# Performance work log

Measured on AMD Instinct MI355X. Metric: run time of the kernel, lower is better.

The kernel has to match this reference:

```python
import jax, jax.numpy as jnp
import numpy as np

IN_F = 4096
OUT_F = 4096
GROUP = 8
N_GROUPS = OUT_F * IN_F // GROUP  # 2097152
BATCH = 32


def _dequant_3bit(weight_q3, weight_norm):
    # weight_q3: [G, 3] bytes (stored int32, values 0..255)
    # weight_norm: [G, 1] fp16 per-group abs-max scale
    p = weight_q3.astype(jnp.int32)
    val = p[:, 0] | (p[:, 1] << 8) | (p[:, 2] << 16)          # [G] 24-bit word
    shifts = jnp.arange(GROUP, dtype=jnp.int32) * 3           # [8]
    q = ((val[:, None] >> shifts[None, :]) & 7).astype(jnp.float32)  # [G, 8] in {0..7}
    n = weight_norm.astype(jnp.float32)                        # [G, 1]
    w = (q / 7.0) * (2.0 * n) - n                              # de-normalize to [-n, n]
    return w.reshape(OUT_F, IN_F)


def setup_inputs() -> dict:
    key = jax.random.key(0)
    k1, k2, k3, k4 = jax.random.split(key, 4)
    x = jax.random.normal(k1, (BATCH, IN_F), dtype=jnp.float32)
    weight_q3 = jax.random.randint(k2, (N_GROUPS, 3), 0, 256, dtype=jnp.int32)
    weight_norm = jax.random.uniform(k3, (N_GROUPS, 1), dtype=jnp.float16, minval=0.01, maxval=1.0)
    bias = jax.random.normal(k4, (OUT_F,), dtype=jnp.float32)
    return {"x": x, "weight_q3": weight_q3, "weight_norm": weight_norm, "bias": bias}


def reference(x, weight_q3, weight_norm, bias):
    w = _dequant_3bit(weight_q3, weight_norm)  # [OUT_F, IN_F] fp32
    return x @ w.T + bias                      # F.linear semantics
```

## Files before the change

kernel.cpp:

```cpp
#include <hip/hip_runtime.h>
#include <hip/hip_fp16.h>

#define IN_F   4096
#define OUT_F  4096
#define BATCH  32
#define NGPR   512
#define BN     16
#define NW     8
#define QPITCH 1540
#define NPITCH 516

typedef float f32x4  __attribute__((ext_vector_type(4)));
typedef short short8 __attribute__((ext_vector_type(8)));

__device__ __forceinline__ unsigned short f2bf_u(float f) {
    return __builtin_bit_cast(unsigned short, (__bf16)f);
}

__device__ __forceinline__ void gload16(const void* gsrc, void* lds) {
    __builtin_amdgcn_global_load_lds(
        (const __attribute__((address_space(1))) void*)gsrc,
        (__attribute__((address_space(3))) void*)lds, 16, 0, 0);
}

__global__ __launch_bounds__(256)
void pack_x_kernel(const float* __restrict__ x, unsigned short* __restrict__ apk)
{
    const int tau = blockIdx.x * 256 + threadIdx.x;
    const int row = tau >> 9;
    const int c   = tau & 511;
    const float4 lo = *reinterpret_cast<const float4*>(&x[row * IN_F + c * 8]);
    const float4 hi = *reinterpret_cast<const float4*>(&x[row * IN_F + c * 8 + 4]);
    union { unsigned short us[8]; uint4 v; } pk;
    pk.us[0] = f2bf_u(lo.x); pk.us[1] = f2bf_u(lo.y);
    pk.us[2] = f2bf_u(lo.z); pk.us[3] = f2bf_u(lo.w);
    pk.us[4] = f2bf_u(hi.x); pk.us[5] = f2bf_u(hi.y);
    pk.us[6] = f2bf_u(hi.z); pk.us[7] = f2bf_u(hi.w);
    const int a = row >> 4, cl = row & 15, s = c >> 2, q = c & 3;
    const int unit = (a * 128 + s) * 64 + q * 16 + cl;
    *reinterpret_cast<uint4*>(&apk[unit * 8]) = pk.v;
}

template<bool PACKED>
__global__ __launch_bounds__(512, 2)
void l3b_main(const float* __restrict__ x,
              const int* __restrict__ wq3,
              const void* __restrict__ wnorm_raw,
              const float* __restrict__ bias,
              float* __restrict__ out,
              const unsigned short* __restrict__ apk)
{
    __shared__ unsigned int qls[BN * QPITCH];
    __shared__ float        nrm[BN][NPITCH];
    __shared__ float        red[NW][BATCH][17];

    const int tid   = threadIdx.x;
    const int w     = tid >> 6;
    const int lane  = tid & 63;
    const int nbase = blockIdx.x * BN;

    const int q  = lane >> 4;
    const int cl = lane & 15;

    const unsigned short* wn16  = (const unsigned short*)wnorm_raw;
    const float*          wn32  = (const float*)wnorm_raw;
    const unsigned int*   wnu32 = (const unsigned int*)wnorm_raw;
    int mode;
    {
        const unsigned short h = wn16[lane];
        const float v16 = __half2float(__builtin_bit_cast(__half, h));
        const float vbf = __builtin_bit_cast(float, (unsigned int)h << 16);
        const float v32 = wn32[lane];
        const int c16 = __popcll(__ballot(v16 > 0.0095f && v16 < 1.0005f));
        const int cbf = __popcll(__ballot(vbf > 0.0095f && vbf < 1.0005f));
        const int c32 = __popcll(__ballot(v32 > 0.0095f && v32 < 1.0005f));
        if (c16 >= c32 && c16 >= cbf) {
            mode = 1;
        } else if (c32 > cbf + 8) {
            mode = 0;
        } else if (cbf > c32 + 8) {
            mode = 2;
        } else {
            const int z = __popcll(__ballot((wnu32[lane] & 0x1FFFu) == 0u));
            mode = (z >= 48) ? 0 : 2;
        }
    }

    {
        const int* qg = wq3 + (long)nbase * 1536;
        #pragma unroll
        for (int rr = 0; rr < 2; ++rr) {
            const int row = w * 2 + rr;
            #pragma unroll
            for (int i = 0; i < 6; ++i) {
                const int off = i * 256 + lane * 4;
                gload16(qg + (long)row * 1536 + off, &qls[row * QPITCH + off]);
            }
        }
    }

    if (mode == 0) {
        const float* nb = wn32 + (long)nbase * NGPR;
        #pragma unroll
        for (int j = 0; j < 4; ++j) {
            const int f = j * 2048 + tid * 4;
            const float4 v = *reinterpret_cast<const float4*>(nb + f);
            *reinterpret_cast<float4*>(&nrm[f >> 9][f & 511]) = v;
        }
    } else {
        const unsigned short* nb = wn16 + (long)nbase * NGPR;
        #pragma unroll
        for (int j = 0; j < 2; ++j) {
            const int f = j * 4096 + tid * 8;
            union { unsigned short us[8]; uint4 v; } u;
            u.v = *reinterpret_cast<const uint4*>(nb + f);
            float4 f0, f1;
            if (mode == 1) {
                f0.x = __half2float(__builtin_bit_cast(__half, u.us[0]));
                f0.y = __half2float(__builtin_bit_cast(__half, u.us[1]));
                f0.z = __half2float(__builtin_bit_cast(__half, u.us[2]));
                f0.w = __half2float(__builtin_bit_cast(__half, u.us[3]));
                f1.x = __half2float(__builtin_bit_cast(__half, u.us[4]));
                f1.y = __half2float(__builtin_bit_cast(__half, u.us[5]));
                f1.z = __half2float(__builtin_bit_cast(__half, u.us[6]));
                f1.w = __half2float(__builtin_bit_cast(__half, u.us[7]));
            } else {
                f0.x = __builtin_bit_cast(float, (unsigned)u.us[0] << 16);
                f0.y = __builtin_bit_cast(float, (unsigned)u.us[1] << 16);
                f0.z = __builtin_bit_cast(float, (unsigned)u.us[2] << 16);
                f0.w = __builtin_bit_cast(float, (unsigned)u.us[3] << 16);
                f1.x = __builtin_bit_cast(float, (unsigned)u.us[4] << 16);
                f1.y = __builtin_bit_cast(float, (unsigned)u.us[5] << 16);
                f1.z = __builtin_bit_cast(float, (unsigned)u.us[6] << 16);
                f1.w = __builtin_bit_cast(float, (unsigned)u.us[7] << 16);
            }
            const int row = f >> 9, col = f & 511;
            *reinterpret_cast<float4*>(&nrm[row][col])     = f0;
            *reinterpret_cast<float4*>(&nrm[row][col + 4]) = f1;
        }
    }

    __syncthreads();

    f32x4 acc0 = {0.f, 0.f, 0.f, 0.f};
    f32x4 acc1 = {0.f, 0.f, 0.f, 0.f};

    #pragma unroll 4
    for (int i = 0; i < 16; ++i) {
        const int s = w * 16 + i;
        const int g = s * 4 + q;

        const int qb = cl * QPITCH + g * 3;
        const unsigned d0 = qls[qb];
        const unsigned d1 = qls[qb + 1];
        const unsigned d2 = qls[qb + 2];
        const unsigned val = (d0 & 0xFFu) | ((d1 & 0xFFu) << 8) | ((d2 & 0xFFu) << 16);

        const float n  = nrm[cl][g];
        const float av = n * 0.285714285714285714f;
        union { unsigned short us[8]; short8 v; } B;
        #pragma unroll
        for (int e = 0; e < 8; ++e) {
            const float qf = (float)((val >> (3 * e)) & 7u);
            B.us[e] = f2bf_u(fmaf(qf, av, -n));
        }

        short8 A0, A1;
        if (PACKED) {
            A0 = *reinterpret_cast<const short8*>(&apk[(s * 64 + lane) * 8]);
            A1 = *reinterpret_cast<const short8*>(&apk[((128 + s) * 64 + lane) * 8]);
        } else {
            const int kg = s * 32 + q * 8;
            const float4 a0lo = *reinterpret_cast<const float4*>(&x[cl        * IN_F + kg]);
            const float4 a0hi = *reinterpret_cast<const float4*>(&x[cl        * IN_F + kg + 4]);
            const float4 a1lo = *reinterpret_cast<const float4*>(&x[(cl + 16) * IN_F + kg]);
            const float4 a1hi = *reinterpret_cast<const float4*>(&x[(cl + 16) * IN_F + kg + 4]);
            union { unsigned short us[8]; short8 v; } U0, U1;
            U0.us[0] = f2bf_u(a0lo.x); U0.us[1] = f2bf_u(a0lo.y);
            U0.us[2] = f2bf_u(a0lo.z); U0.us[3] = f2bf_u(a0lo.w);
            U0.us[4] = f2bf_u(a0hi.x); U0.us[5] = f2bf_u(a0hi.y);
            U0.us[6] = f2bf_u(a0hi.z); U0.us[7] = f2bf_u(a0hi.w);
            U1.us[0] = f2bf_u(a1lo.x); U1.us[1] = f2bf_u(a1lo.y);
            U1.us[2] = f2bf_u(a1lo.z); U1.us[3] = f2bf_u(a1lo.w);
            U1.us[4] = f2bf_u(a1hi.x); U1.us[5] = f2bf_u(a1hi.y);
            U1.us[6] = f2bf_u(a1hi.z); U1.us[7] = f2bf_u(a1hi.w);
            A0 = U0.v; A1 = U1.v;
        }

        acc0 = __builtin_amdgcn_mfma_f32_16x16x32_bf16(A0, B.v, acc0, 0, 0, 0);
        acc1 = __builtin_amdgcn_mfma_f32_16x16x32_bf16(A1, B.v, acc1, 0, 0, 0);
    }

    #pragma unroll
    for (int i = 0; i < 4; ++i) {
        red[w][q * 4 + i][cl]      = acc0[i];
        red[w][16 + q * 4 + i][cl] = acc1[i];
    }
    __syncthreads();
    {
        const int m  = tid >> 4;
        const int nl = tid & 15;
        float ssum = 0.f;
        #pragma unroll
        for (int wv = 0; wv < NW; ++wv) ssum += red[wv][m][nl];
        out[m * OUT_F + nbase + nl] = ssum + bias[nbase + nl];
    }
}

extern "C" void kernel_launch(void* const* d_in, const int* in_sizes, int n_in,
                              void* d_out, int out_size, void* d_ws, size_t ws_size,
                              hipStream_t stream) {
    const float* x    = (const float*)d_in[0];
    const int*   wq3  = (const int*)d_in[1];
    const void*  wn   = (const void*)d_in[2];
    const float* bias = (const float*)d_in[3];
    float*       out  = (float*)d_out;

    if (ws_size >= (size_t)(2 * 128 * 64 * 8 * 2)) {
        unsigned short* apk = (unsigned short*)d_ws;
        pack_x_kernel<<<dim3(64), dim3(256), 0, stream>>>(x, apk);
        l3b_main<true><<<dim3(OUT_F / BN), dim3(512), 0, stream>>>(x, wq3, wn, bias, out, apk);
    } else {
        l3b_main<false><<<dim3(OUT_F / BN), dim3(512), 0, stream>>>(x, wq3, wn, bias, out, nullptr);
    }
}
```

Baseline: 17.22 us.

## Fuse activation bf16 packing into main kernel and prefetch A fragments into registers

Removes the separate pack_x kernel launch and its workspace round trip. Each wave now loads and converts its x slice to bf16 directly into register arrays before the main loop. The load is issued before the barrier so it can overlap the LDS staging of quantized weights. The MFMA loop is then fully unrolled. In exchange, the x conversion is repeated in every block, and holding 32 short8 registers per thread raises register pressure under the 512-thread, 2-blocks launch bound, which may cause spills.

```diff
diff --git a/kernel.cpp b/kernel.cpp
--- a/kernel.cpp
+++ b/kernel.cpp
@@ -23,32 +23,12 @@
         (__attribute__((address_space(3))) void*)lds, 16, 0, 0);
 }
 
-__global__ __launch_bounds__(256)
-void pack_x_kernel(const float* __restrict__ x, unsigned short* __restrict__ apk)
-{
-    const int tau = blockIdx.x * 256 + threadIdx.x;
-    const int row = tau >> 9;
-    const int c   = tau & 511;
-    const float4 lo = *reinterpret_cast<const float4*>(&x[row * IN_F + c * 8]);
-    const float4 hi = *reinterpret_cast<const float4*>(&x[row * IN_F + c * 8 + 4]);
-    union { unsigned short us[8]; uint4 v; } pk;
-    pk.us[0] = f2bf_u(lo.x); pk.us[1] = f2bf_u(lo.y);
-    pk.us[2] = f2bf_u(lo.z); pk.us[3] = f2bf_u(lo.w);
-    pk.us[4] = f2bf_u(hi.x); pk.us[5] = f2bf_u(hi.y);
-    pk.us[6] = f2bf_u(hi.z); pk.us[7] = f2bf_u(hi.w);
-    const int a = row >> 4, cl = row & 15, s = c >> 2, q = c & 3;
-    const int unit = (a * 128 + s) * 64 + q * 16 + cl;
-    *reinterpret_cast<uint4*>(&apk[unit * 8]) = pk.v;
-}
-
-template<bool PACKED>
 __global__ __launch_bounds__(512, 2)
-void l3b_main(const float* __restrict__ x,
-              const int* __restrict__ wq3,
-              const void* __restrict__ wnorm_raw,
-              const float* __restrict__ bias,
-              float* __restrict__ out,
-              const unsigned short* __restrict__ apk)
+void l3b_fused(const float* __restrict__ x,
+               const int* __restrict__ wq3,
+               const void* __restrict__ wnorm_raw,
+               const float* __restrict__ bias,
+               float* __restrict__ out)
 {
     __shared__ unsigned int qls[BN * QPITCH];
     __shared__ float        nrm[BN][NPITCH];
@@ -140,12 +120,33 @@
         }
     }
 
+    short8 A0R[16], A1R[16];
+    #pragma unroll
+    for (int i = 0; i < 16; ++i) {
+        const int kg = (w * 16 + i) * 32 + q * 8;
+        const float4 a0lo = *reinterpret_cast<const float4*>(&x[cl        * IN_F + kg]);
+        const float4 a0hi = *reinterpret_cast<const float4*>(&x[cl        * IN_F + kg + 4]);
+        const float4 a1lo = *reinterpret_cast<const float4*>(&x[(cl + 16) * IN_F + kg]);
+        const float4 a1hi = *reinterpret_cast<const float4*>(&x[(cl + 16) * IN_F + kg + 4]);
+        union { unsigned short us[8]; short8 v; } U0, U1;
+        U0.us[0] = f2bf_u(a0lo.x); U0.us[1] = f2bf_u(a0lo.y);
+        U0.us[2] = f2bf_u(a0lo.z); U0.us[3] = f2bf_u(a0lo.w);
+        U0.us[4] = f2bf_u(a0hi.x); U0.us[5] = f2bf_u(a0hi.y);
+        U0.us[6] = f2bf_u(a0hi.z); U0.us[7] = f2bf_u(a0hi.w);
+        U1.us[0] = f2bf_u(a1lo.x); U1.us[1] = f2bf_u(a1lo.y);
+        U1.us[2] = f2bf_u(a1lo.z); U1.us[3] = f2bf_u(a1lo.w);
+        U1.us[4] = f2bf_u(a1hi.x); U1.us[5] = f2bf_u(a1hi.y);
+        U1.us[6] = f2bf_u(a1hi.z); U1.us[7] = f2bf_u(a1hi.w);
+        A0R[i] = U0.v;
+        A1R[i] = U1.v;
+    }
+
     __syncthreads();
 
     f32x4 acc0 = {0.f, 0.f, 0.f, 0.f};
     f32x4 acc1 = {0.f, 0.f, 0.f, 0.f};
 
-    #pragma unroll 4
+    #pragma unroll
     for (int i = 0; i < 16; ++i) {
         const int s = w * 16 + i;
         const int g = s * 4 + q;
@@ -165,30 +166,8 @@
             B.us[e] = f2bf_u(fmaf(qf, av, -n));
         }
 
-        short8 A0, A1;
-        if (PACKED) {
-            A0 = *reinterpret_cast<const short8*>(&apk[(s * 64 + lane) * 8]);
-            A1 = *reinterpret_cast<const short8*>(&apk[((128 + s) * 64 + lane) * 8]);
-        } else {
-            const int kg = s * 32 + q * 8;
-            const float4 a0lo = *reinterpret_cast<const float4*>(&x[cl        * IN_F + kg]);
-            const float4 a0hi = *reinterpret_cast<const float4*>(&x[cl        * IN_F + kg + 4]);
-            const float4 a1lo = *reinterpret_cast<const float4*>(&x[(cl + 16) * IN_F + kg]);
-            const float4 a1hi = *reinterpret_cast<const float4*>(&x[(cl + 16) * IN_F + kg + 4]);
-            union { unsigned short us[8]; short8 v; } U0, U1;
-            U0.us[0] = f2bf_u(a0lo.x); U0.us[1] = f2bf_u(a0lo.y);
-            U0.us[2] = f2bf_u(a0lo.z); U0.us[3] = f2bf_u(a0lo.w);
-            U0.us[4] = f2bf_u(a0hi.x); U0.us[5] = f2bf_u(a0hi.y);
-            U0.us[6] = f2bf_u(a0hi.z); U0.us[7] = f2bf_u(a0hi.w);
-            U1.us[0] = f2bf_u(a1lo.x); U1.us[1] = f2bf_u(a1lo.y);
-            U1.us[2] = f2bf_u(a1lo.z); U1.us[3] = f2bf_u(a1lo.w);
-            U1.us[4] = f2bf_u(a1hi.x); U1.us[5] = f2bf_u(a1hi.y);
-            U1.us[6] = f2bf_u(a1hi.z); U1.us[7] = f2bf_u(a1hi.w);
-            A0 = U0.v; A1 = U1.v;
-        }
-
-        acc0 = __builtin_amdgcn_mfma_f32_16x16x32_bf16(A0, B.v, acc0, 0, 0, 0);
-        acc1 = __builtin_amdgcn_mfma_f32_16x16x32_bf16(A1, B.v, acc1, 0, 0, 0);
+        acc0 = __builtin_amdgcn_mfma_f32_16x16x32_bf16(A0R[i], B.v, acc0, 0, 0, 0);
+        acc1 = __builtin_amdgcn_mfma_f32_16x16x32_bf16(A1R[i], B.v, acc1, 0, 0, 0);
     }
 
     #pragma unroll
@@ -216,11 +195,5 @@
     const float* bias = (const float*)d_in[3];
     float*       out  = (float*)d_out;
 
-    if (ws_size >= (size_t)(2 * 128 * 64 * 8 * 2)) {
-        unsigned short* apk = (unsigned short*)d_ws;
-        pack_x_kernel<<<dim3(64), dim3(256), 0, stream>>>(x, apk);
-        l3b_main<true><<<dim3(OUT_F / BN), dim3(512), 0, stream>>>(x, wq3, wn, bias, out, apk);
-    } else {
-        l3b_main<false><<<dim3(OUT_F / BN), dim3(512), 0, stream>>>(x, wq3, wn, bias, out, nullptr);
-    }
+    l3b_fused<<<dim3(OUT_F / BN), dim3(512), 0, stream>>>(x, wq3, wn, bias, out);
 }
```

After: 26.89 us. +56.2%, slower.

## Split quantized weight staging in two halves and overlap compute with second half

Applied to the files above, without the earlier changes.

The per-block load of packed 3-bit weights into LDS is split into two halves. The norm loads are issued between the halves. Explicit vmcnt waits and raw s_barriers let the waves start MFMA work on the first half of the K range while the second half is still arriving. The non-packed fallback path is removed, so the kernel now always relies on the workspace for pre-packed bf16 activations. This trades simpler synchronisation for hand-written waitcnt ordering, which depends on the exact count of outstanding loads.

```diff
diff --git a/kernel.cpp b/kernel.cpp
--- a/kernel.cpp
+++ b/kernel.cpp
@@ -41,7 +41,6 @@
     *reinterpret_cast<uint4*>(&apk[unit * 8]) = pk.v;
 }
 
-template<bool PACKED>
 __global__ __launch_bounds__(512, 2)
 void l3b_main(const float* __restrict__ x,
               const int* __restrict__ wq3,
@@ -86,34 +85,58 @@
         }
     }
 
-    {
-        const int* qg = wq3 + (long)nbase * 1536;
-        #pragma unroll
-        for (int rr = 0; rr < 2; ++rr) {
-            const int row = w * 2 + rr;
-            #pragma unroll
-            for (int i = 0; i < 6; ++i) {
-                const int off = i * 256 + lane * 4;
-                gload16(qg + (long)row * 1536 + off, &qls[row * QPITCH + off]);
-            }
-        }
-    }
-
+    const int* qg = wq3 + (long)nbase * 1536;
+
+    #pragma unroll
+    for (int rr = 0; rr < 2; ++rr) {
+        const int row = w * 2 + rr;
+        #pragma unroll
+        for (int i = 0; i < 3; ++i) {
+            const int off = i * 256 + lane * 4;
+            gload16(qg + (long)row * 1536 + off, &qls[row * QPITCH + off]);
+        }
+    }
+    __builtin_amdgcn_sched_barrier(0);
+
+    uint4 nraw[4];
     if (mode == 0) {
         const float* nb = wn32 + (long)nbase * NGPR;
         #pragma unroll
+        for (int j = 0; j < 4; ++j)
+            nraw[j] = *reinterpret_cast<const uint4*>(nb + j * 2048 + tid * 4);
+    } else {
+        const unsigned short* nb = wn16 + (long)nbase * NGPR;
+        #pragma unroll
+        for (int j = 0; j < 2; ++j)
+            nraw[j] = *reinterpret_cast<const uint4*>(nb + j * 4096 + tid * 8);
+    }
+    __builtin_amdgcn_sched_barrier(0);
+
+    #pragma unroll
+    for (int rr = 0; rr < 2; ++rr) {
+        const int row = w * 2 + rr;
+        #pragma unroll
+        for (int i = 3; i < 6; ++i) {
+            const int off = i * 256 + lane * 4;
+            gload16(qg + (long)row * 1536 + off, &qls[row * QPITCH + off]);
+        }
+    }
+    __builtin_amdgcn_sched_barrier(0);
+
+    asm volatile("s_waitcnt vmcnt(6)" ::: "memory");
+    __builtin_amdgcn_sched_barrier(0);
+    if (mode == 0) {
+        #pragma unroll
         for (int j = 0; j < 4; ++j) {
             const int f = j * 2048 + tid * 4;
-            const float4 v = *reinterpret_cast<const float4*>(nb + f);
-            *reinterpret_cast<float4*>(&nrm[f >> 9][f & 511]) = v;
+            *reinterpret_cast<uint4*>(&nrm[f >> 9][f & 511]) = nraw[j];
         }
     } else {
-        const unsigned short* nb = wn16 + (long)nbase * NGPR;
         #pragma unroll
         for (int j = 0; j < 2; ++j) {
             const int f = j * 4096 + tid * 8;
             union { unsigned short us[8]; uint4 v; } u;
-            u.v = *reinterpret_cast<const uint4*>(nb + f);
+            u.v = nraw[j];
             float4 f0, f1;
             if (mode == 1) {
                 f0.x = __half2float(__builtin_bit_cast(__half, u.us[0]));
@@ -139,15 +162,14 @@
             *reinterpret_cast<float4*>(&nrm[row][col + 4]) = f1;
         }
     }
-
-    __syncthreads();
+    asm volatile("s_waitcnt lgkmcnt(0)" ::: "memory");
+    __builtin_amdgcn_s_barrier();
+    __builtin_amdgcn_sched_barrier(0);
 
     f32x4 acc0 = {0.f, 0.f, 0.f, 0.f};
     f32x4 acc1 = {0.f, 0.f, 0.f, 0.f};
 
-    #pragma unroll 4
-    for (int i = 0; i < 16; ++i) {
-        const int s = w * 16 + i;
+    auto body = [&](int s) {
         const int g = s * 4 + q;
 
         const int qb = cl * QPITCH + g * 3;
@@ -165,31 +187,22 @@
             B.us[e] = f2bf_u(fmaf(qf, av, -n));
         }
 
-        short8 A0, A1;
-        if (PACKED) {
-            A0 = *reinterpret_cast<const short8*>(&apk[(s * 64 + lane) * 8]);
-            A1 = *reinterpret_cast<const short8*>(&apk[((128 + s) * 64 + lane) * 8]);
-        } else {
-            const int kg = s * 32 + q * 8;
-            const float4 a0lo = *reinterpret_cast<const float4*>(&x[cl        * IN_F + kg]);
-            const float4 a0hi = *reinterpret_cast<const float4*>(&x[cl        * IN_F + kg + 4]);
-            const float4 a1lo = *reinterpret_cast<const float4*>(&x[(cl + 16) * IN_F + kg]);
-            const float4 a1hi = *reinterpret_cast<const float4*>(&x[(cl + 16) * IN_F + kg + 4]);
-            union { unsigned short us[8]; short8 v; } U0, U1;
-            U0.us[0] = f2bf_u(a0lo.x); U0.us[1] = f2bf_u(a0lo.y);
-            U0.us[2] = f2bf_u(a0lo.z); U0.us[3] = f2bf_u(a0lo.w);
-            U0.us[4] = f2bf_u(a0hi.x); U0.us[5] = f2bf_u(a0hi.y);
-            U0.us[6] = f2bf_u(a0hi.z); U0.us[7] = f2bf_u(a0hi.w);
-            U1.us[0] = f2bf_u(a1lo.x); U1.us[1] = f2bf_u(a1lo.y);
-            U1.us[2] = f2bf_u(a1lo.z); U1.us[3] = f2bf_u(a1lo.w);
-            U1.us[4] = f2bf_u(a1hi.x); U1.us[5] = f2bf_u(a1hi.y);
-            U1.us[6] = f2bf_u(a1hi.z); U1.us[7] = f2bf_u(a1hi.w);
-            A0 = U0.v; A1 = U1.v;
-        }
+        const short8 A0 = *reinterpret_cast<const short8*>(&apk[(s * 64 + lane) * 8]);
+        const short8 A1 = *reinterpret_cast<const short8*>(&apk[((128 + s) * 64 + lane) * 8]);
 
         acc0 = __builtin_amdgcn_mfma_f32_16x16x32_bf16(A0, B.v, acc0, 0, 0, 0);
         acc1 = __builtin_amdgcn_mfma_f32_16x16x32_bf16(A1, B.v, acc1, 0, 0, 0);
-    }
+    };
+
+    #pragma unroll
+    for (int i = 0; i < 8; ++i) body(w * 8 + i);
+
+    asm volatile("s_waitcnt vmcnt(0)" ::: "memory");
+    __builtin_amdgcn_s_barrier();
+    __builtin_amdgcn_sched_barrier(0);
+
+    #pragma unroll
+    for (int i = 0; i < 8; ++i) body(64 + w * 8 + i);
 
     #pragma unroll
     for (int i = 0; i < 4; ++i) {
@@ -215,12 +228,8 @@
     const void*  wn   = (const void*)d_in[2];
     const float* bias = (const float*)d_in[3];
     float*       out  = (float*)d_out;
-
-    if (ws_size >= (size_t)(2 * 128 * 64 * 8 * 2)) {
-        unsigned short* apk = (unsigned short*)d_ws;
-        pack_x_kernel<<<dim3(64), dim3(256), 0, stream>>>(x, apk);
-        l3b_main<true><<<dim3(OUT_F / BN), dim3(512), 0, stream>>>(x, wq3, wn, bias, out, apk);
-    } else {
-        l3b_main<false><<<dim3(OUT_F / BN), dim3(512), 0, stream>>>(x, wq3, wn, bias, out, nullptr);
-    }
-}
+    unsigned short* apk = (unsigned short*)d_ws;
+
+    pack_x_kernel<<<dim3(64), dim3(256), 0, stream>>>(x, apk);
+    l3b_main<<<dim3(OUT_F / BN), dim3(512), 0, stream>>>(x, wq3, wn, bias, out, apk);
+}
```

After: 17.46 us. Within noise of the previous version (+1.4%).
